# Performance work log

Measured on AMD Instinct MI355X. Metric: run time of the kernel, lower is better.

Reference implementation:

```python
import jax, jax.numpy as jnp
import numpy as np
import math

D, H, NQP, NKP = 512, 8, 4, 4
DH = D // H
OUT_DIM = D + H * NKP * 3  # 608


def setup_inputs() -> dict:
    key = jax.random.key(0)
    ks = jax.random.split(key, 12)
    B, L = 2, 1024
    s = jax.random.normal(ks[0], (B, L, D), dtype=jnp.float32)
    R = jax.random.normal(ks[1], (B, L, 3, 3), dtype=jnp.float32)
    tr = jax.random.normal(ks[2], (B, L, 3), dtype=jnp.float32)
    sc = 0.02
    Wq = jax.random.normal(ks[3], (D, D), dtype=jnp.float32) * sc
    Wk = jax.random.normal(ks[4], (D, D), dtype=jnp.float32) * sc
    Wv = jax.random.normal(ks[5], (D, D), dtype=jnp.float32) * sc
    Wqp = jax.random.normal(ks[6], (D, H * NQP * 3), dtype=jnp.float32) * sc
    Wkp = jax.random.normal(ks[7], (D, H * NKP * 3), dtype=jnp.float32) * sc
    Wvp = jax.random.normal(ks[8], (D, H * NKP * 3), dtype=jnp.float32) * sc
    Wo = jax.random.normal(ks[9], (OUT_DIM, D), dtype=jnp.float32) * sc
    bo = jnp.zeros((D,), dtype=jnp.float32)
    gamma = jnp.ones((D,), dtype=jnp.float32)
    beta = jnp.zeros((D,), dtype=jnp.float32)
    w_C = jnp.full((H,), math.log(20.0), dtype=jnp.float32)
    return dict(s=s, R=R, tr=tr, Wq=Wq, Wk=Wk, Wv=Wv, Wqp=Wqp, Wkp=Wkp,
                Wvp=Wvp, Wo=Wo, bo=bo, gamma=gamma, beta=beta, w_C=w_C)


def _layernorm(x, gamma, beta, eps=1e-5):
    mu = jnp.mean(x, axis=-1, keepdims=True)
    var = jnp.var(x, axis=-1, keepdims=True)
    return (x - mu) * jax.lax.rsqrt(var + eps) * gamma + beta


def reference(s, R, tr, Wq, Wk, Wv, Wqp, Wkp, Wvp, Wo, bo, gamma, beta, w_C):
    B, L, _ = s.shape
    # scalar q/k/v: (B, L, H, dh)
    Q = (s @ Wq).reshape(B, L, H, DH)
    K = (s @ Wk).reshape(B, L, H, DH)
    V = (s @ Wv).reshape(B, L, H, DH)
    a_s = jnp.einsum('bihd,bjhd->bhij', Q, K) / math.sqrt(DH)
    # local points: (B, L, H, P, 3)
    Qp = (s @ Wqp).reshape(B, L, H, NQP, 3)
    Kp = (s @ Wkp).reshape(B, L, H, NKP, 3)
    Vp = (s @ Wvp).reshape(B, L, H, NKP, 3)
    tr_e = tr[:, :, None, None, :]
    to_global = lambda p: jnp.einsum('blxy,blhpy->blhpx', R, p) + tr_e
    Qp_g, Kp_g, Vp_g = to_global(Qp), to_global(Kp), to_global(Vp)
    # (B, H, L, P, 3)
    qh = jnp.transpose(Qp_g, (0, 2, 1, 3, 4))
    kh = jnp.transpose(Kp_g, (0, 2, 1, 3, 4))
    diff = qh[:, :, :, None] - kh[:, :, None]          # (B,H,L,L,P,3)
    sq_dist = jnp.sum(diff * diff, axis=(-2, -1))      # (B,H,L,L)
    wc = jax.nn.softplus(w_C)[None, :, None, None]
    attn = jax.nn.softmax(a_s - 0.5 * wc * sq_dist, axis=-1)
    out_s = jnp.einsum('bhij,bjhd->bihd', attn, V).reshape(B, L, D)
    Vp_agg = jnp.einsum('bhij,bjhpc->bihpc', attn, Vp_g)  # (B,L,H,P,3)
    # global -> local: R^T (p - tr)
    Vp_local = jnp.einsum('blyx,blhpy->blhpx', R, Vp_agg - tr_e)
    out_p = Vp_local.reshape(B, L, H * NKP * 3)
    out = jnp.concatenate([out_s, out_p], axis=-1) @ Wo + bo
    return _layernorm(s + out, gamma, beta)
```

## Files before the change

### kernel.cpp

```cpp
#include <hip/hip_runtime.h>
#include <hip/hip_fp16.h>
#include <math.h>

typedef _Float16 f16;
typedef _Float16 f16x8 __attribute__((ext_vector_type(8)));
typedef _Float16 f16x4v __attribute__((ext_vector_type(4)));
typedef float f32x4 __attribute__((ext_vector_type(4)));

#define BATCH   2
#define LSEQ    1024
#define BLTOT   2048
#define DMODEL  512
#define NHEAD   8
#define PDIM    1824
#define AW      96
#define VW      80
#define ODIM    608
#define NSPLIT  2
#define OCPSTR  1310720

__global__ __launch_bounds__(256)
void prep_kernel(const float* __restrict__ Wq, const float* __restrict__ Wk,
                 const float* __restrict__ Wv, const float* __restrict__ Wqp,
                 const float* __restrict__ Wkp, const float* __restrict__ Wvp,
                 f16* __restrict__ WallT)
{
    const int blk = blockIdx.x;
    const int t = threadIdx.x;
    __shared__ float tile[32][33];

    const int n0 = (blk % 57) * 32, k0 = (blk / 57) * 32;
    const float* src; int ld, nc0;
    if      (n0 < 512)  { src = Wq;  ld = 512; nc0 = n0; }
    else if (n0 < 1024) { src = Wk;  ld = 512; nc0 = n0 - 512; }
    else if (n0 < 1536) { src = Wv;  ld = 512; nc0 = n0 - 1024; }
    else if (n0 < 1632) { src = Wqp; ld = 96;  nc0 = n0 - 1536; }
    else if (n0 < 1728) { src = Wkp; ld = 96;  nc0 = n0 - 1632; }
    else                { src = Wvp; ld = 96;  nc0 = n0 - 1728; }
#pragma unroll
    for (int i = 0; i < 4; ++i) {
        const int idx2 = t + i * 256;
        const int kl = idx2 >> 5, nl = idx2 & 31;
        tile[kl][nl] = src[(long long)(k0 + kl) * ld + nc0 + nl];
    }
    __syncthreads();
#pragma unroll
    for (int i = 0; i < 4; ++i) {
        const int idx2 = t + i * 256;
        const int nl = idx2 >> 5, kl = idx2 & 31;
        WallT[(long long)(n0 + nl) * 512 + k0 + kl] = (f16)tile[kl][nl];
    }
}

__global__ __launch_bounds__(256)
void proj_kernel(const float* __restrict__ S, const f16* __restrict__ Bt,
                 const float* __restrict__ Wo, f16* __restrict__ WoT,
                 f16* __restrict__ P)
{
    __shared__ f16 As[2][64][40];
    __shared__ f16 Bs[2][96][40];
    const int t = threadIdx.x;

    if (blockIdx.y >= 32) {
        float (*tile)[33] = (float(*)[33])&As[0][0][0];
        const int base = (blockIdx.x + (blockIdx.y - 32) * 19) * 8;
#pragma unroll 1
        for (int it = 0; it < 8; ++it) {
            const int idx = base + it;
            const int n0 = (idx & 15) * 32, k0 = (idx >> 4) * 32;
#pragma unroll
            for (int i = 0; i < 4; ++i) {
                const int idx2 = t + i * 256;
                const int kl = idx2 >> 5, nl = idx2 & 31;
                tile[kl][nl] = Wo[(long long)(k0 + kl) * 512 + n0 + nl];
            }
            __syncthreads();
#pragma unroll
            for (int i = 0; i < 4; ++i) {
                const int idx2 = t + i * 256;
                const int nl = idx2 >> 5, kl = idx2 & 31;
                WoT[(long long)(n0 + nl) * 608 + k0 + kl] = (f16)tile[kl][nl];
            }
            __syncthreads();
        }
        return;
    }

    const int w = t >> 6, lane = t & 63, l15 = lane & 15, lhi = lane >> 4;
    const int row0 = blockIdx.y * 64, col0 = blockIdx.x * 96;
    const int ar = t >> 2, ac = t & 3;
    const int K = 512;

    f32x4 acc[6];
#pragma unroll
    for (int n = 0; n < 6; ++n) acc[n] = (f32x4){0.f, 0.f, 0.f, 0.f};

    float4 a0, a1;
    f16x8 bR[2];
    a0 = *(const float4*)&S[(long long)(row0 + ar) * K + ac * 8];
    a1 = *(const float4*)&S[(long long)(row0 + ar) * K + ac * 8 + 4];
#pragma unroll
    for (int i = 0; i < 2; ++i) {
        const int cid = t + i * 256;
        if (cid < 384) {
            const int br = cid >> 2, bc = cid & 3;
            bR[i] = *(const f16x8*)&Bt[(long long)(col0 + br) * K + bc * 8];
        }
    }
    {
        f16x8 v = { (f16)a0.x, (f16)a0.y, (f16)a0.z, (f16)a0.w,
                    (f16)a1.x, (f16)a1.y, (f16)a1.z, (f16)a1.w };
        *(f16x8*)&As[0][ar][ac * 8] = v;
    }
#pragma unroll
    for (int i = 0; i < 2; ++i) {
        const int cid = t + i * 256;
        if (cid < 384) *(f16x8*)&Bs[0][cid >> 2][(cid & 3) * 8] = bR[i];
    }
    __syncthreads();

    for (int st = 0; st < 16; ++st) {
        const int cur = st & 1;
        if (st + 1 < 16) {
            const int k0 = (st + 1) << 5;
            a0 = *(const float4*)&S[(long long)(row0 + ar) * K + k0 + ac * 8];
            a1 = *(const float4*)&S[(long long)(row0 + ar) * K + k0 + ac * 8 + 4];
#pragma unroll
            for (int i = 0; i < 2; ++i) {
                const int cid = t + i * 256;
                if (cid < 384) {
                    const int br = cid >> 2, bc = cid & 3;
                    bR[i] = *(const f16x8*)&Bt[(long long)(col0 + br) * K + k0 + bc * 8];
                }
            }
        }
        f16x8 af = *(const f16x8*)&As[cur][w * 16 + l15][lhi * 8];
        f16x8 bf[6];
#pragma unroll
        for (int n = 0; n < 6; ++n)
            bf[n] = *(const f16x8*)&Bs[cur][n * 16 + l15][lhi * 8];
#pragma unroll
        for (int n = 0; n < 6; ++n)
            acc[n] = __builtin_amdgcn_mfma_f32_16x16x32_f16(af, bf[n], acc[n], 0, 0, 0);
        if (st + 1 < 16) {
            f16x8 v = { (f16)a0.x, (f16)a0.y, (f16)a0.z, (f16)a0.w,
                        (f16)a1.x, (f16)a1.y, (f16)a1.z, (f16)a1.w };
            *(f16x8*)&As[cur ^ 1][ar][ac * 8] = v;
#pragma unroll
            for (int i = 0; i < 2; ++i) {
                const int cid = t + i * 256;
                if (cid < 384) *(f16x8*)&Bs[cur ^ 1][cid >> 2][(cid & 3) * 8] = bR[i];
            }
        }
        __syncthreads();
    }

    const int row = row0 + w * 16 + lhi * 4;
#pragma unroll
    for (int n = 0; n < 6; ++n) {
        const int col = col0 + n * 16 + l15;
#pragma unroll
        for (int r = 0; r < 4; ++r)
            P[(long long)(row + r) * PDIM + col] = (f16)acc[n][r];
    }
}

template<int BN, bool OUT16>
__global__ __launch_bounds__(256)
void gemm2_kernel(const f16* __restrict__ A, const f16* __restrict__ Bt,
                  void* __restrict__ Cout, int K, int ldc)
{
    constexpr int BCH = (BN * 4 + 255) / 256;
    __shared__ f16 As[2][64][40];
    __shared__ f16 Bs[2][BN][40];
    const int t = threadIdx.x;
    const int w = t >> 6, lane = t & 63, l15 = lane & 15, lhi = lane >> 4;
    const int row0 = blockIdx.y * 64, col0 = blockIdx.x * BN;
    const int ar = t >> 2, ac = t & 3;

    f32x4 acc[BN / 16];
#pragma unroll
    for (int n = 0; n < BN / 16; ++n) acc[n] = (f32x4){0.f, 0.f, 0.f, 0.f};

    const int nsteps = K >> 5;

    f16x8 aR;
    f16x8 bR[BCH];
    aR = *(const f16x8*)&A[(long long)(row0 + ar) * K + ac * 8];
#pragma unroll
    for (int i = 0; i < BCH; ++i) {
        const int cid = t + i * 256;
        if (cid < BN * 4) {
            const int br = cid >> 2, bc = cid & 3;
            bR[i] = *(const f16x8*)&Bt[(long long)(col0 + br) * K + bc * 8];
        }
    }
    *(f16x8*)&As[0][ar][ac * 8] = aR;
#pragma unroll
    for (int i = 0; i < BCH; ++i) {
        const int cid = t + i * 256;
        if (cid < BN * 4) *(f16x8*)&Bs[0][cid >> 2][(cid & 3) * 8] = bR[i];
    }
    __syncthreads();

    for (int st = 0; st < nsteps; ++st) {
        const int cur = st & 1;
        if (st + 1 < nsteps) {
            const int k0 = (st + 1) << 5;
            aR = *(const f16x8*)&A[(long long)(row0 + ar) * K + k0 + ac * 8];
#pragma unroll
            for (int i = 0; i < BCH; ++i) {
                const int cid = t + i * 256;
                if (cid < BN * 4) {
                    const int br = cid >> 2, bc = cid & 3;
                    bR[i] = *(const f16x8*)&Bt[(long long)(col0 + br) * K + k0 + bc * 8];
                }
            }
        }
        f16x8 af = *(const f16x8*)&As[cur][w * 16 + l15][lhi * 8];
        f16x8 bf[BN / 16];
#pragma unroll
        for (int n = 0; n < BN / 16; ++n)
            bf[n] = *(const f16x8*)&Bs[cur][n * 16 + l15][lhi * 8];
#pragma unroll
        for (int n = 0; n < BN / 16; ++n)
            acc[n] = __builtin_amdgcn_mfma_f32_16x16x32_f16(af, bf[n], acc[n], 0, 0, 0);
        if (st + 1 < nsteps) {
            *(f16x8*)&As[cur ^ 1][ar][ac * 8] = aR;
#pragma unroll
            for (int i = 0; i < BCH; ++i) {
                const int cid = t + i * 256;
                if (cid < BN * 4) *(f16x8*)&Bs[cur ^ 1][cid >> 2][(cid & 3) * 8] = bR[i];
            }
        }
        __syncthreads();
    }

    const int row = row0 + w * 16 + lhi * 4;
#pragma unroll
    for (int n = 0; n < BN / 16; ++n) {
        const int col = col0 + n * 16 + l15;
#pragma unroll
        for (int r = 0; r < 4; ++r) {
            if (OUT16) ((f16*)Cout)[(long long)(row + r) * ldc + col] = (f16)acc[n][r];
            else       ((float*)Cout)[(long long)(row + r) * ldc + col] = acc[n][r];
        }
    }
}

__global__ __launch_bounds__(256)
void build_aug2_kernel(const f16* __restrict__ P, const float* __restrict__ Rm,
                       const float* __restrict__ tr, const float* __restrict__ wC,
                       f16* __restrict__ QA, f16* __restrict__ KA,
                       f16* __restrict__ VCT)
{
    const int l0 = blockIdx.x * 64;
    const int bh = blockIdx.y;
    const int b = bh >> 3, h = bh & 7;
    const int t = threadIdx.x;

    __shared__ float Rl[64][9];
    __shared__ float trl[64][3];
    __shared__ f16 gq[64][12];
    __shared__ f16 gk[64][12];
    __shared__ float k2[64][4];
    __shared__ f16 Vt[VW][72];
    __shared__ float wcs;

    const long long blbase = (long long)b * LSEQ + l0;

    for (int i = t; i < 64 * 9; i += 256) Rl[i / 9][i % 9] = Rm[blbase * 9 + i];
    for (int i = t; i < 64 * 3; i += 256) trl[i / 3][i % 3] = tr[blbase * 3 + i];
    if (t == 0) { float x = wC[h]; wcs = log1pf(expf(x)); }
    __syncthreads();
    const float wc = wcs;

    for (int i = t; i < 768; i += 256) {
        const int l = i / 12, pp = i - l * 12;
        const int proj = pp >> 2, p = pp & 3;
        const f16* src = P + (blbase + l) * PDIM + 1536 + proj * 96 + h * 12 + p * 3;
        const float x = (float)src[0], y = (float)src[1], z = (float)src[2];
        const float gx = Rl[l][0]*x + Rl[l][1]*y + Rl[l][2]*z + trl[l][0];
        const float gy = Rl[l][3]*x + Rl[l][4]*y + Rl[l][5]*z + trl[l][1];
        const float gz = Rl[l][6]*x + Rl[l][7]*y + Rl[l][8]*z + trl[l][2];
        if (proj == 0) {
            gq[l][p * 3 + 0] = (f16)(wc * gx);
            gq[l][p * 3 + 1] = (f16)(wc * gy);
            gq[l][p * 3 + 2] = (f16)(wc * gz);
        } else if (proj == 1) {
            gk[l][p * 3 + 0] = (f16)gx;
            gk[l][p * 3 + 1] = (f16)gy;
            gk[l][p * 3 + 2] = (f16)gz;
            k2[l][p] = gx * gx + gy * gy + gz * gz;
        } else {
            Vt[64 + p * 3 + 0][l] = (f16)gx;
            Vt[64 + p * 3 + 1][l] = (f16)gy;
            Vt[64 + p * 3 + 2][l] = (f16)gz;
        }
    }
    for (int i = t; i < 512; i += 256) {
        const int l = i >> 3, ch = i & 7;
        f16x8 v = *(const f16x8*)&P[(blbase + l) * PDIM + 1024 + h * 64 + ch * 8];
#pragma unroll
        for (int j = 0; j < 8; ++j) Vt[ch * 8 + j][l] = v[j];
    }
    for (int i = t; i < 36; i += 256) {
        const int r = 76 + i / 9, ch = i % 9;
        *(f16x8*)&Vt[r][ch * 8] = (f16x8){0,0,0,0,0,0,0,0};
    }
    __syncthreads();

    for (int i = t; i < 768; i += 256) {
        const int l = i / 12, ch = i - l * 12;
        const long long prow = (blbase + l) * PDIM;
        const long long orow = ((long long)bh * LSEQ + l0 + l) * AW;
        f16x8 q, k;
        if (ch < 8) {
            f16x8 qv = *(const f16x8*)&P[prow + h * 64 + ch * 8];
            f16x8 kv = *(const f16x8*)&P[prow + 512 + h * 64 + ch * 8];
            q = qv * (f16)0.125f;
            k = kv;
        } else if (ch == 8) {
#pragma unroll
            for (int j = 0; j < 8; ++j) { q[j] = gq[l][j]; k[j] = gk[l][j]; }
        } else if (ch == 9) {
            const float koff = 0.5f * wc * (k2[l][0] + k2[l][1] + k2[l][2] + k2[l][3]);
            const f16 kh = (f16)koff;
            const float kres = koff - (float)kh;
#pragma unroll
            for (int j = 0; j < 4; ++j) { q[j] = gq[l][8 + j]; k[j] = gk[l][8 + j]; }
            q[4] = (f16)1.f; k[4] = -kh;
            q[5] = (f16)1.f; k[5] = (f16)(-kres);
            q[6] = (f16)0.f; k[6] = (f16)0.f;
            q[7] = (f16)0.f; k[7] = (f16)0.f;
        } else {
            q = (f16x8){0,0,0,0,0,0,0,0};
            k = (f16x8){0,0,0,0,0,0,0,0};
        }
        *(f16x8*)&QA[orow + ch * 8] = q;
        *(f16x8*)&KA[orow + ch * 8] = k;
    }
    for (int i = t; i < 640; i += 256) {
        const int c = i >> 3, lg = i & 7;
        *(f16x8*)&VCT[((long long)bh * VW + c) * LSEQ + l0 + lg * 8] =
            *(const f16x8*)&Vt[c][lg * 8];
    }
}

__global__ __launch_bounds__(256, 2)
void attn_kernel(const f16* __restrict__ QA, const f16* __restrict__ KA,
                 const f16* __restrict__ VCT,
                 f16* __restrict__ OCp, float* __restrict__ LSE)
{
    const int bh = blockIdx.y;
    const int q0 = blockIdx.x * 64;
    const int z  = blockIdx.z;
    const int t = threadIdx.x;
    const int w = t >> 6, lane = t & 63, l15 = lane & 15, lhi = lane >> 4;

    __shared__ f16 Ks[128][104];
    __shared__ f16 Vs[VW][136];
    __shared__ f16 Ps[64][136];

    const f16* qbase = QA + ((long long)bh * LSEQ + q0 + w * 16 + l15) * AW;
    f16x8 qf[3];
#pragma unroll
    for (int ks = 0; ks < 3; ++ks)
        qf[ks] = *(const f16x8*)(qbase + ks * 32 + lhi * 8);

    f32x4 Oacc[5];
#pragma unroll
    for (int nv = 0; nv < 5; ++nv) Oacc[nv] = (f32x4){0.f, 0.f, 0.f, 0.f};
    float M = -1e30f, L = 0.f;

    const f16* kgbase = KA + (long long)bh * LSEQ * AW;
    const f16* vgbase = VCT + (long long)bh * VW * LSEQ;

    const int kvbeg = z * (LSEQ / NSPLIT);
    const int kvend = kvbeg + LSEQ / NSPLIT;

#pragma unroll
    for (int i = 0; i < 6; ++i) {
        const int cid = t + i * 256;
        const int r = cid / 12, c = cid - r * 12;
        *(f16x8*)&Ks[r][c * 8] = *(const f16x8*)(kgbase + (long long)(kvbeg + r) * AW + c * 8);
    }
#pragma unroll
    for (int i = 0; i < 5; ++i) {
        const int cid = t + i * 256;
        const int r = cid >> 4, c = cid & 15;
        *(f16x8*)&Vs[r][c * 8] = *(const f16x8*)(vgbase + (long long)r * LSEQ + kvbeg + c * 8);
    }
    __syncthreads();

    for (int kv0 = kvbeg; kv0 < kvend; kv0 += 128) {
        const bool more = (kv0 + 128 < kvend);
        f16x8 kpre[6], vpre[5];
        if (more) {
#pragma unroll
            for (int i = 0; i < 6; ++i) {
                const int cid = t + i * 256;
                const int r = cid / 12, c = cid - r * 12;
                kpre[i] = *(const f16x8*)(kgbase + (long long)(kv0 + 128 + r) * AW + c * 8);
            }
#pragma unroll
            for (int i = 0; i < 5; ++i) {
                const int cid = t + i * 256;
                const int r = cid >> 4, c = cid & 15;
                vpre[i] = *(const f16x8*)(vgbase + (long long)r * LSEQ + kv0 + 128 + c * 8);
            }
        }

        f32x4 sc[8];
#pragma unroll
        for (int n = 0; n < 8; ++n) sc[n] = (f32x4){0.f, 0.f, 0.f, 0.f};
        __builtin_amdgcn_s_setprio(1);
#pragma unroll
        for (int n = 0; n < 8; ++n)
#pragma unroll
            for (int ks = 0; ks < 3; ++ks) {
                f16x8 kb = *(const f16x8*)&Ks[n * 16 + l15][ks * 32 + lhi * 8];
                sc[n] = __builtin_amdgcn_mfma_f32_16x16x32_f16(kb, qf[ks], sc[n], 0, 0, 0);
            }
        __builtin_amdgcn_s_setprio(0);

        float mr = sc[0][0];
#pragma unroll
        for (int n = 0; n < 8; ++n)
#pragma unroll
            for (int r = 0; r < 4; ++r) mr = fmaxf(mr, sc[n][r]);
        mr = fmaxf(mr, __shfl_xor(mr, 16));
        mr = fmaxf(mr, __shfl_xor(mr, 32));

        const bool nog = (mr <= M + 8.f);
        float rsum = 0.f;
        if (__all(nog)) {
#pragma unroll
            for (int n = 0; n < 8; ++n)
#pragma unroll
                for (int r = 0; r < 4; ++r) {
                    const float p = __expf(sc[n][r] - M);
                    sc[n][r] = p;
                    rsum += p;
                }
            rsum += __shfl_xor(rsum, 16);
            rsum += __shfl_xor(rsum, 32);
            L += rsum;
        } else {
            const float nm = fmaxf(M, mr);
            const float ss = __expf(M - nm);
            M = nm;
#pragma unroll
            for (int n = 0; n < 8; ++n)
#pragma unroll
                for (int r = 0; r < 4; ++r) {
                    const float p = __expf(sc[n][r] - M);
                    sc[n][r] = p;
                    rsum += p;
                }
            rsum += __shfl_xor(rsum, 16);
            rsum += __shfl_xor(rsum, 32);
            L = L * ss + rsum;
            float sr[4];
#pragma unroll
            for (int r = 0; r < 4; ++r) sr[r] = __shfl(ss, lhi * 4 + r);
#pragma unroll
            for (int nv = 0; nv < 5; ++nv)
#pragma unroll
                for (int r = 0; r < 4; ++r) Oacc[nv][r] *= sr[r];
        }

#pragma unroll
        for (int n = 0; n < 8; ++n) {
            f16x4v pv = { (f16)sc[n][0], (f16)sc[n][1], (f16)sc[n][2], (f16)sc[n][3] };
            *(f16x4v*)&Ps[w * 16 + l15][n * 16 + lhi * 4] = pv;
        }

        f16x8 pa[4];
#pragma unroll
        for (int ks = 0; ks < 4; ++ks)
            pa[ks] = *(const f16x8*)&Ps[w * 16 + l15][ks * 32 + lhi * 8];
        __builtin_amdgcn_s_setprio(1);
#pragma unroll
        for (int nv = 0; nv < 5; ++nv)
#pragma unroll
            for (int ks = 0; ks < 4; ++ks) {
                f16x8 vb = *(const f16x8*)&Vs[nv * 16 + l15][ks * 32 + lhi * 8];
                Oacc[nv] = __builtin_amdgcn_mfma_f32_16x16x32_f16(pa[ks], vb, Oacc[nv], 0, 0, 0);
            }
        __builtin_amdgcn_s_setprio(0);
        __syncthreads();

        if (more) {
#pragma unroll
            for (int i = 0; i < 6; ++i) {
                const int cid = t + i * 256;
                const int r = cid / 12, c = cid - r * 12;
                *(f16x8*)&Ks[r][c * 8] = kpre[i];
            }
#pragma unroll
            for (int i = 0; i < 5; ++i) {
                const int cid = t + i * 256;
                const int r = cid >> 4, c = cid & 15;
                *(f16x8*)&Vs[r][c * 8] = vpre[i];
            }
        }
        __syncthreads();
    }

    float invr[4];
#pragma unroll
    for (int r = 0; r < 4; ++r) {
        const float Lr = __shfl(L, lhi * 4 + r);
        invr[r] = 1.0f / Lr;
    }
    f16* obase = OCp + (((long long)(z * 16 + bh) * LSEQ) + q0 + w * 16 + lhi * 4) * VW;
#pragma unroll
    for (int nv = 0; nv < 5; ++nv)
#pragma unroll
        for (int r = 0; r < 4; ++r)
            obase[r * VW + nv * 16 + l15] = (f16)(Oacc[nv][r] * invr[r]);
    if (lhi == 0) {
        LSE[(long long)(z * 16 + bh) * LSEQ + q0 + w * 16 + l15] = M + __logf(L);
    }
}

__global__ __launch_bounds__(256)
void combine_concat_kernel(const f16* __restrict__ OCp, const float* __restrict__ LSE,
                           const float* __restrict__ Rm, const float* __restrict__ tr,
                           f16* __restrict__ CC)
{
    const int bl0 = blockIdx.x * 4;
    const int b = bl0 >> 10;
    const int t = threadIdx.x;

    __shared__ float w1s[4][8], w2s[4][8];
    if (t < 32) {
        const int row = t >> 3, h = t & 7;
        const int l = (bl0 + row) & 1023;
        const int bh = b * 8 + h;
        const float l1 = LSE[(long long)bh * LSEQ + l];
        const float l2 = LSE[(long long)(16 + bh) * LSEQ + l];
        const float mm = fmaxf(l1, l2);
        const float e1 = __expf(l1 - mm), e2 = __expf(l2 - mm);
        const float inv = 1.0f / (e1 + e2);
        w1s[row][h] = e1 * inv; w2s[row][h] = e2 * inv;
    }
    __syncthreads();

    for (int idx = t; idx < 2048; idx += 256) {
        const int row = idx >> 9, c = idx & 511;
        const int h = c >> 6, ch = c & 63;
        const int l = (bl0 + row) & 1023;
        const long long base = ((long long)(b * 8 + h) * LSEQ + l) * VW + ch;
        const float v = w1s[row][h] * (float)OCp[base] + w2s[row][h] * (float)OCp[OCPSTR + base];
        CC[(long long)(bl0 + row) * ODIM + c] = (f16)v;
    }
    if (t < 128) {
        const int row = t >> 5, h = (t >> 2) & 7, p = t & 3;
        const int bl = bl0 + row, l = bl & 1023;
        const long long base = ((long long)(b * 8 + h) * LSEQ + l) * VW + 64 + p * 3;
        const float w1 = w1s[row][h], w2 = w2s[row][h];
        float o[3];
#pragma unroll
        for (int c = 0; c < 3; ++c)
            o[c] = w1 * (float)OCp[base + c] + w2 * (float)OCp[OCPSTR + base + c]
                 - tr[(long long)bl * 3 + c];
        const float* Rr = Rm + (long long)bl * 9;
        f16* crow = CC + (long long)bl * ODIM + 512 + h * 12 + p * 3;
        crow[0] = (f16)(Rr[0]*o[0] + Rr[3]*o[1] + Rr[6]*o[2]);
        crow[1] = (f16)(Rr[1]*o[0] + Rr[4]*o[1] + Rr[7]*o[2]);
        crow[2] = (f16)(Rr[2]*o[0] + Rr[5]*o[1] + Rr[8]*o[2]);
    }
}

__global__ __launch_bounds__(256)
void residual_ln_kernel(const float* __restrict__ s, const float* __restrict__ Y,
                        const float* __restrict__ bo, const float* __restrict__ gamma,
                        const float* __restrict__ beta, float* __restrict__ out)
{
    const int bl = blockIdx.x;
    const int t = threadIdx.x;
    const float* srow = s + (long long)bl * DMODEL;
    const float* yrow = Y + (long long)bl * DMODEL;

    const float v0 = srow[t]       + yrow[t]       + bo[t];
    const float v1 = srow[t + 256] + yrow[t + 256] + bo[t + 256];

    float sum = v0 + v1, sq = v0 * v0 + v1 * v1;
#pragma unroll
    for (int o = 32; o > 0; o >>= 1) {
        sum += __shfl_xor(sum, o);
        sq  += __shfl_xor(sq,  o);
    }
    __shared__ float rs[4], rq[4];
    const int wid = t >> 6, lane = t & 63;
    if (lane == 0) { rs[wid] = sum; rq[wid] = sq; }
    __syncthreads();
    sum = rs[0] + rs[1] + rs[2] + rs[3];
    sq  = rq[0] + rq[1] + rq[2] + rq[3];

    const float mu  = sum * (1.0f / DMODEL);
    const float var = sq * (1.0f / DMODEL) - mu * mu;
    const float inv = rsqrtf(var + 1e-5f);

    out[(long long)bl * DMODEL + t]       = (v0 - mu) * inv * gamma[t]       + beta[t];
    out[(long long)bl * DMODEL + t + 256] = (v1 - mu) * inv * gamma[t + 256] + beta[t + 256];
}

extern "C" void kernel_launch(void* const* d_in, const int* in_sizes, int n_in,
                              void* d_out, int out_size, void* d_ws, size_t ws_size,
                              hipStream_t stream)
{
    const float* s    = (const float*)d_in[0];
    const float* R    = (const float*)d_in[1];
    const float* tr   = (const float*)d_in[2];
    const float* Wq   = (const float*)d_in[3];
    const float* Wk   = (const float*)d_in[4];
    const float* Wv   = (const float*)d_in[5];
    const float* Wqp  = (const float*)d_in[6];
    const float* Wkp  = (const float*)d_in[7];
    const float* Wvp  = (const float*)d_in[8];
    const float* Wo   = (const float*)d_in[9];
    const float* bo   = (const float*)d_in[10];
    const float* gam  = (const float*)d_in[11];
    const float* bet  = (const float*)d_in[12];
    const float* wC   = (const float*)d_in[13];
    float* out = (float*)d_out;

    f16* WallT = (f16*)d_ws;
    f16* WoT   = WallT + 933888;
    f16* P     = WoT + 311296;
    f16* QA    = P + 3735552;
    f16* KA    = QA + 1572864;
    f16* VCT   = KA + 1572864;
    f16* OCp   = VCT + 1310720;
    float* LSE = (float*)(OCp + 2621440);
    f16* CC    = (f16*)(LSE + 32768);
    float* Y   = (float*)(CC + 1245184);

    const dim3 blk(256);

    prep_kernel<<<dim3(912), blk, 0, stream>>>(Wq, Wk, Wv, Wqp, Wkp, Wvp, WallT);

    proj_kernel<<<dim3(19, 34), blk, 0, stream>>>(s, WallT, Wo, WoT, P);

    build_aug2_kernel<<<dim3(16, 16), blk, 0, stream>>>(P, R, tr, wC, QA, KA, VCT);

    attn_kernel<<<dim3(16, 16, NSPLIT), blk, 0, stream>>>(QA, KA, VCT, OCp, LSE);

    combine_concat_kernel<<<dim3(512), blk, 0, stream>>>(OCp, LSE, R, tr, CC);

    gemm2_kernel<64, false><<<dim3(8, 32), blk, 0, stream>>>(CC, WoT, Y, 608, 512);

    residual_ln_kernel<<<dim3(BLTOT), blk, 0, stream>>>(s, Y, bo, gam, bet, out);
}
```

Measured before the change: 70.73 us.

## Split attention KV tile across wave pairs with two query subtiles per wave

Each wave now handles 32 query rows, as two 16-row MFMA subtiles, over half of the 128-key tile. The other half is handled by a partner wave, so each K and V fragment read from LDS feeds two MFMAs. At the end the two halves' partial softmax states (M, L, O) are merged through shared memory, reusing the Ks buffer. This cuts LDS traffic per MFMA but doubles accumulator registers and adds an extra barrier plus a combine step at the epilogue.

```diff
diff --git a/kernel.cpp b/kernel.cpp
--- a/kernel.cpp
+++ b/kernel.cpp
@@ -357,21 +357,28 @@
     const int z  = blockIdx.z;
     const int t = threadIdx.x;
     const int w = t >> 6, lane = t & 63, l15 = lane & 15, lhi = lane >> 4;
+    const int wsub = w & 1;
+    const int kh   = w >> 1;
 
     __shared__ f16 Ks[128][104];
     __shared__ f16 Vs[VW][136];
     __shared__ f16 Ps[64][136];
 
-    const f16* qbase = QA + ((long long)bh * LSEQ + q0 + w * 16 + l15) * AW;
-    f16x8 qf[3];
-#pragma unroll
-    for (int ks = 0; ks < 3; ++ks)
-        qf[ks] = *(const f16x8*)(qbase + ks * 32 + lhi * 8);
-
-    f32x4 Oacc[5];
-#pragma unroll
-    for (int nv = 0; nv < 5; ++nv) Oacc[nv] = (f32x4){0.f, 0.f, 0.f, 0.f};
-    float M = -1e30f, L = 0.f;
+    f16x8 qf[2][3];
+#pragma unroll
+    for (int m = 0; m < 2; ++m) {
+        const f16* qb = QA + ((long long)bh * LSEQ + q0 + wsub * 32 + m * 16 + l15) * AW;
+#pragma unroll
+        for (int ks = 0; ks < 3; ++ks)
+            qf[m][ks] = *(const f16x8*)(qb + ks * 32 + lhi * 8);
+    }
+
+    f32x4 Oacc[2][5];
+#pragma unroll
+    for (int m = 0; m < 2; ++m)
+#pragma unroll
+        for (int nv = 0; nv < 5; ++nv) Oacc[m][nv] = (f32x4){0.f, 0.f, 0.f, 0.f};
+    float M[2] = {-1e30f, -1e30f}, L[2] = {0.f, 0.f};
 
     const f16* kgbase = KA + (long long)bh * LSEQ * AW;
     const f16* vgbase = VCT + (long long)bh * VW * LSEQ;
@@ -411,82 +418,104 @@
             }
         }
 
-        f32x4 sc[8];
-#pragma unroll
-        for (int n = 0; n < 8; ++n) sc[n] = (f32x4){0.f, 0.f, 0.f, 0.f};
+        f32x4 sc[2][4];
+#pragma unroll
+        for (int m = 0; m < 2; ++m)
+#pragma unroll
+            for (int n = 0; n < 4; ++n) sc[m][n] = (f32x4){0.f, 0.f, 0.f, 0.f};
         __builtin_amdgcn_s_setprio(1);
 #pragma unroll
-        for (int n = 0; n < 8; ++n)
+        for (int n = 0; n < 4; ++n)
 #pragma unroll
             for (int ks = 0; ks < 3; ++ks) {
-                f16x8 kb = *(const f16x8*)&Ks[n * 16 + l15][ks * 32 + lhi * 8];
-                sc[n] = __builtin_amdgcn_mfma_f32_16x16x32_f16(kb, qf[ks], sc[n], 0, 0, 0);
+                f16x8 kb = *(const f16x8*)&Ks[kh * 64 + n * 16 + l15][ks * 32 + lhi * 8];
+                sc[0][n] = __builtin_amdgcn_mfma_f32_16x16x32_f16(kb, qf[0][ks], sc[0][n], 0, 0, 0);
+                sc[1][n] = __builtin_amdgcn_mfma_f32_16x16x32_f16(kb, qf[1][ks], sc[1][n], 0, 0, 0);
             }
         __builtin_amdgcn_s_setprio(0);
 
-        float mr = sc[0][0];
-#pragma unroll
-        for (int n = 0; n < 8; ++n)
-#pragma unroll
-            for (int r = 0; r < 4; ++r) mr = fmaxf(mr, sc[n][r]);
-        mr = fmaxf(mr, __shfl_xor(mr, 16));
-        mr = fmaxf(mr, __shfl_xor(mr, 32));
-
-        const bool nog = (mr <= M + 8.f);
-        float rsum = 0.f;
+        float mr[2];
+#pragma unroll
+        for (int m = 0; m < 2; ++m) {
+            float mm = sc[m][0][0];
+#pragma unroll
+            for (int n = 0; n < 4; ++n)
+#pragma unroll
+                for (int r = 0; r < 4; ++r) mm = fmaxf(mm, sc[m][n][r]);
+            mm = fmaxf(mm, __shfl_xor(mm, 16));
+            mm = fmaxf(mm, __shfl_xor(mm, 32));
+            mr[m] = mm;
+        }
+        const bool nog = (mr[0] <= M[0] + 8.f) && (mr[1] <= M[1] + 8.f);
         if (__all(nog)) {
 #pragma unroll
-            for (int n = 0; n < 8; ++n)
+            for (int m = 0; m < 2; ++m) {
+                float rsum = 0.f;
+#pragma unroll
+                for (int n = 0; n < 4; ++n)
+#pragma unroll
+                    for (int r = 0; r < 4; ++r) {
+                        const float p = __expf(sc[m][n][r] - M[m]);
+                        sc[m][n][r] = p;
+                        rsum += p;
+                    }
+                rsum += __shfl_xor(rsum, 16);
+                rsum += __shfl_xor(rsum, 32);
+                L[m] += rsum;
+            }
+        } else {
+            float ss[2];
+#pragma unroll
+            for (int m = 0; m < 2; ++m) {
+                const float nm = fmaxf(M[m], mr[m]);
+                ss[m] = __expf(M[m] - nm);
+                M[m] = nm;
+                float rsum = 0.f;
+#pragma unroll
+                for (int n = 0; n < 4; ++n)
+#pragma unroll
+                    for (int r = 0; r < 4; ++r) {
+                        const float p = __expf(sc[m][n][r] - M[m]);
+                        sc[m][n][r] = p;
+                        rsum += p;
+                    }
+                rsum += __shfl_xor(rsum, 16);
+                rsum += __shfl_xor(rsum, 32);
+                L[m] = L[m] * ss[m] + rsum;
+            }
+#pragma unroll
+            for (int m = 0; m < 2; ++m)
 #pragma unroll
                 for (int r = 0; r < 4; ++r) {
-                    const float p = __expf(sc[n][r] - M);
-                    sc[n][r] = p;
-                    rsum += p;
+                    const float sr = __shfl(ss[m], lhi * 4 + r);
+#pragma unroll
+                    for (int nv = 0; nv < 5; ++nv) Oacc[m][nv][r] *= sr;
                 }
-            rsum += __shfl_xor(rsum, 16);
-            rsum += __shfl_xor(rsum, 32);
-            L += rsum;
-        } else {
-            const float nm = fmaxf(M, mr);
-            const float ss = __expf(M - nm);
-            M = nm;
-#pragma unroll
-            for (int n = 0; n < 8; ++n)
-#pragma unroll
-                for (int r = 0; r < 4; ++r) {
-                    const float p = __expf(sc[n][r] - M);
-                    sc[n][r] = p;
-                    rsum += p;
-                }
-            rsum += __shfl_xor(rsum, 16);
-            rsum += __shfl_xor(rsum, 32);
-            L = L * ss + rsum;
-            float sr[4];
-#pragma unroll
-            for (int r = 0; r < 4; ++r) sr[r] = __shfl(ss, lhi * 4 + r);
-#pragma unroll
-            for (int nv = 0; nv < 5; ++nv)
-#pragma unroll
-                for (int r = 0; r < 4; ++r) Oacc[nv][r] *= sr[r];
-        }
-
-#pragma unroll
-        for (int n = 0; n < 8; ++n) {
-            f16x4v pv = { (f16)sc[n][0], (f16)sc[n][1], (f16)sc[n][2], (f16)sc[n][3] };
-            *(f16x4v*)&Ps[w * 16 + l15][n * 16 + lhi * 4] = pv;
-        }
-
-        f16x8 pa[4];
-#pragma unroll
-        for (int ks = 0; ks < 4; ++ks)
-            pa[ks] = *(const f16x8*)&Ps[w * 16 + l15][ks * 32 + lhi * 8];
+        }
+
+#pragma unroll
+        for (int m = 0; m < 2; ++m)
+#pragma unroll
+            for (int n = 0; n < 4; ++n) {
+                f16x4v pv = { (f16)sc[m][n][0], (f16)sc[m][n][1],
+                              (f16)sc[m][n][2], (f16)sc[m][n][3] };
+                *(f16x4v*)&Ps[wsub * 32 + m * 16 + l15][kh * 64 + n * 16 + lhi * 4] = pv;
+            }
+
+        f16x8 pa[2][2];
+#pragma unroll
+        for (int m = 0; m < 2; ++m)
+#pragma unroll
+            for (int k2i = 0; k2i < 2; ++k2i)
+                pa[m][k2i] = *(const f16x8*)&Ps[wsub * 32 + m * 16 + l15][kh * 64 + k2i * 32 + lhi * 8];
         __builtin_amdgcn_s_setprio(1);
 #pragma unroll
         for (int nv = 0; nv < 5; ++nv)
 #pragma unroll
-            for (int ks = 0; ks < 4; ++ks) {
-                f16x8 vb = *(const f16x8*)&Vs[nv * 16 + l15][ks * 32 + lhi * 8];
-                Oacc[nv] = __builtin_amdgcn_mfma_f32_16x16x32_f16(pa[ks], vb, Oacc[nv], 0, 0, 0);
+            for (int k2i = 0; k2i < 2; ++k2i) {
+                f16x8 vb = *(const f16x8*)&Vs[nv * 16 + l15][kh * 64 + k2i * 32 + lhi * 8];
+                Oacc[0][nv] = __builtin_amdgcn_mfma_f32_16x16x32_f16(pa[0][k2i], vb, Oacc[0][nv], 0, 0, 0);
+                Oacc[1][nv] = __builtin_amdgcn_mfma_f32_16x16x32_f16(pa[1][k2i], vb, Oacc[1][nv], 0, 0, 0);
             }
         __builtin_amdgcn_s_setprio(0);
         __syncthreads();
@@ -508,20 +537,44 @@
         __syncthreads();
     }
 
-    float invr[4];
-#pragma unroll
-    for (int r = 0; r < 4; ++r) {
-        const float Lr = __shfl(L, lhi * 4 + r);
-        invr[r] = 1.0f / Lr;
-    }
-    f16* obase = OCp + (((long long)(z * 16 + bh) * LSEQ) + q0 + w * 16 + lhi * 4) * VW;
-#pragma unroll
-    for (int nv = 0; nv < 5; ++nv)
-#pragma unroll
-        for (int r = 0; r < 4; ++r)
-            obase[r * VW + nv * 16 + l15] = (f16)(Oacc[nv][r] * invr[r]);
-    if (lhi == 0) {
-        LSE[(long long)(z * 16 + bh) * LSEQ + q0 + w * 16 + l15] = M + __logf(L);
+    float* O1  = (float*)&Ks[0][0];
+    float* ML1 = O1 + 64 * 84;
+    if (kh == 1) {
+#pragma unroll
+        for (int m = 0; m < 2; ++m) {
+#pragma unroll
+            for (int nv = 0; nv < 5; ++nv)
+#pragma unroll
+                for (int r = 0; r < 4; ++r)
+                    O1[(wsub * 32 + m * 16 + lhi * 4 + r) * 84 + nv * 16 + l15] = Oacc[m][nv][r];
+            if (lhi == 0) {
+                ML1[(wsub * 32 + m * 16 + l15) * 2 + 0] = M[m];
+                ML1[(wsub * 32 + m * 16 + l15) * 2 + 1] = L[m];
+            }
+        }
+    }
+    __syncthreads();
+    if (kh == 0) {
+#pragma unroll
+        for (int m = 0; m < 2; ++m)
+#pragma unroll
+            for (int r = 0; r < 4; ++r) {
+                const int i = wsub * 32 + m * 16 + lhi * 4 + r;
+                const float Mo = __shfl(M[m], lhi * 4 + r);
+                const float Lo = __shfl(L[m], lhi * 4 + r);
+                const float M1 = ML1[i * 2], L1v = ML1[i * 2 + 1];
+                const float nm = fmaxf(Mo, M1);
+                const float a0 = __expf(Mo - nm), a1 = __expf(M1 - nm);
+                const float Lt = Lo * a0 + L1v * a1;
+                const float inv = 1.0f / Lt;
+                f16* orow = OCp + (((long long)(z * 16 + bh) * LSEQ) + q0 + i) * VW;
+#pragma unroll
+                for (int nv = 0; nv < 5; ++nv)
+                    orow[nv * 16 + l15] =
+                        (f16)((Oacc[m][nv][r] * a0 + O1[i * 84 + nv * 16 + l15] * a1) * inv);
+                if (l15 == 0)
+                    LSE[(long long)(z * 16 + bh) * LSEQ + q0 + i] = nm + __logf(Lt);
+            }
     }
 }
 
```

Result: slower. 90.26 us (+27.6%).
